# Performance work log

Hardware: AMD Instinct MI355X
Metric: run time of the kernel (lower is better)

The kernel has to match this reference:

```python
import jax, jax.numpy as jnp
import numpy as np

N_NODES = 100000
N_EDGES = 1600000
N_ROOTS = 2048


def _with_self_loops(edge_index, num_nodes):
    loop = jnp.arange(num_nodes, dtype=edge_index.dtype)
    src = jnp.concatenate([edge_index[0], loop])
    dst = jnp.concatenate([edge_index[1], loop])
    return src, dst


def gcn_conv(x, w, b, src, dst, num_nodes):
    xw = x @ w  # [N, Fout]
    deg = jax.ops.segment_sum(jnp.ones_like(dst, dtype=xw.dtype), dst,
                              num_segments=num_nodes)
    dinv = jnp.where(deg > 0, jax.lax.rsqrt(jnp.maximum(deg, 1.0)) * (deg > 0), 0.0)
    dinv = jnp.where(deg > 0, deg ** -0.5, 0.0)
    norm = dinv[src] * dinv[dst]  # [E+N]
    msgs = norm[:, None] * xw[src]  # [E+N, Fout] -- dominant memory traffic
    out = jax.ops.segment_sum(msgs, dst, num_segments=num_nodes)
    return out + b


def setup_inputs() -> dict:
    key = jax.random.key(0)
    ks = jax.random.split(key, 10)
    x = jax.random.normal(ks[0], (N_NODES, 256), dtype=jnp.float32)
    edge_index = jax.random.randint(ks[1], (2, N_EDGES), 0, N_NODES, dtype=jnp.int32)
    bu_edge_index = jax.random.randint(ks[2], (2, N_EDGES), 0, N_NODES, dtype=jnp.int32)
    rootindex = jax.random.randint(ks[3], (N_ROOTS,), 0, N_NODES, dtype=jnp.int32)
    def glorot(k, shape):
        lim = (6.0 / (shape[0] + shape[1])) ** 0.5
        return jax.random.uniform(k, shape, jnp.float32, -lim, lim)
    return {
        "x": x, "edge_index": edge_index, "bu_edge_index": bu_edge_index,
        "rootindex": rootindex,
        "w1": glorot(ks[4], (256, 128)), "b1": jnp.zeros((128,), jnp.float32),
        "w2": glorot(ks[5], (128, 128)), "b2": jnp.zeros((128,), jnp.float32),
        "w3": glorot(ks[6], (256, 128)), "b3": jnp.zeros((128,), jnp.float32),
        "w4": glorot(ks[7], (128, 128)), "b4": jnp.zeros((128,), jnp.float32),
        "fc_w": glorot(ks[8], (256, 4)), "fc_b": jnp.zeros((4,), jnp.float32),
    }


def reference(x, edge_index, bu_edge_index, rootindex,
              w1, b1, w2, b2, w3, b3, w4, b4, fc_w, fc_b):
    n = x.shape[0]
    src_td, dst_td = _with_self_loops(edge_index, n)
    src_bu, dst_bu = _with_self_loops(bu_edge_index, n)

    # Top-down branch (dropout is identity in eval mode)
    h = jax.nn.elu(gcn_conv(x, w1, b1, src_td, dst_td, n))
    h = jax.nn.elu(gcn_conv(h, w2, b2, src_td, dst_td, n))
    h = h[rootindex]  # [B, 128]

    # Bottom-up branch
    h1 = jax.nn.elu(gcn_conv(x, w3, b3, src_bu, dst_bu, n))
    h1 = jax.nn.elu(gcn_conv(h1, w4, b4, src_bu, dst_bu, n))
    h1 = h1[rootindex]  # [B, 128]

    feat = jnp.concatenate([h, h1], axis=1)  # [B, 256]
    logits = feat @ fc_w + fc_b  # [B, 4]
    return jax.nn.log_softmax(logits, axis=1)
```

## Files before the change

### kernel.cpp

```cpp
#include <hip/hip_runtime.h>
#include <hip/hip_fp16.h>
#include <math.h>

typedef __attribute__((ext_vector_type(8))) short short8v;
typedef __attribute__((ext_vector_type(4))) float float4v;
typedef __attribute__((ext_vector_type(4))) unsigned short ushort4v;
typedef __attribute__((ext_vector_type(8))) unsigned short ushort8v;

#define CH 4096
#define MAXNB 800

__device__ inline unsigned short f2bf(float f) {
    unsigned u = __float_as_uint(f);
    return (unsigned short)((u + 0x7FFFu + ((u >> 16) & 1u)) >> 16);
}


__global__ __launch_bounds__(256) void bin1_kernel(const int* __restrict__ dst, int E, int NB,
                                                   int* __restrict__ gcnt,
                                                   int* __restrict__ blockBase) {
    __shared__ int h[MAXNB];
    int t = threadIdx.x;
    for (int i = t; i < NB; i += 256) h[i] = 0;
    __syncthreads();
    int e0 = blockIdx.x * CH;
#pragma unroll
    for (int i = 0; i < CH / 256; ++i) {
        int e = e0 + t + i * 256;
        if (e < E) atomicAdd(&h[dst[e] >> 7], 1);
    }
    __syncthreads();
    for (int b = t; b < NB; b += 256) {
        int c = h[b];
        int old = atomicAdd(&gcnt[b], c);
        blockBase[(size_t)blockIdx.x * MAXNB + b] = old;
    }
}


__global__ void scan1_kernel(const int* __restrict__ cnt, int N,
                             int* __restrict__ offs) {
    __shared__ int sd[256];
    int t = threadIdx.x;
    int base = t * 4;
    int v[4]; int s = 0;
#pragma unroll
    for (int i = 0; i < 4; ++i) { v[i] = (base + i < N) ? cnt[base + i] : 0; s += v[i]; }
    sd[t] = s; __syncthreads();
    for (int d = 1; d < 256; d <<= 1) {
        int x = (t >= d) ? sd[t - d] : 0;
        __syncthreads();
        sd[t] += x;
        __syncthreads();
    }
    int p = sd[t] - s;
#pragma unroll
    for (int i = 0; i < 4; ++i) { if (base + i < N) offs[base + i] = p; p += v[i]; }
}


__global__ __launch_bounds__(256) void bin2_kernel(const int* __restrict__ src,
                                                   const int* __restrict__ dst, int E, int NB,
                                                   const int* __restrict__ boff,
                                                   const int* __restrict__ blockBase,
                                                   int* __restrict__ ebuf) {
    __shared__ int h[MAXNB];
    __shared__ int intra[MAXNB];
    __shared__ int cursor[MAXNB];
    __shared__ int gbase[MAXNB];
    __shared__ int ps[256];
    __shared__ int sorted[CH];
    __shared__ unsigned char sbkt[CH];
    int t = threadIdx.x;
    int blk = blockIdx.x;
    for (int i = t; i < NB; i += 256) h[i] = 0;
    __syncthreads();
    int e0 = blk * CH;
#pragma unroll
    for (int i = 0; i < CH / 256; ++i) {
        int e = e0 + t + i * 256;
        if (e < E) atomicAdd(&h[dst[e] >> 7], 1);
    }
    __syncthreads();
    int base4 = t * 4;
    int v[4]; int s = 0;
#pragma unroll
    for (int k = 0; k < 4; ++k) { v[k] = (base4 + k < NB) ? h[base4 + k] : 0; s += v[k]; }
    ps[t] = s; __syncthreads();
    for (int d = 1; d < 256; d <<= 1) {
        int x = (t >= d) ? ps[t - d] : 0;
        __syncthreads();
        ps[t] += x;
        __syncthreads();
    }
    int p = ps[t] - s;
#pragma unroll
    for (int k = 0; k < 4; ++k) { if (base4 + k < NB) intra[base4 + k] = p; p += v[k]; }
    __syncthreads();
    for (int b = t; b < NB; b += 256) {
        cursor[b] = intra[b];
        gbase[b] = boff[b] + blockBase[(size_t)blk * MAXNB + b] - intra[b];
    }
    __syncthreads();
#pragma unroll
    for (int i = 0; i < CH / 256; ++i) {
        int e = e0 + t + i * 256;
        if (e < E) {
            int d = dst[e];
            int b = d >> 7;
            int pos = atomicAdd(&cursor[b], 1);
            sorted[pos] = (src[e] << 7) | (d & 127);
            sbkt[pos] = (unsigned char)(b & 255);
        }
    }
    __syncthreads();
    int lim = E - e0; if (lim > CH) lim = CH;
    for (int i = t; i < lim; i += 256) {
        int pr = sorted[i];
        int lo = 0, hi = NB - 1;
        while (lo < hi) {
            int mid = (lo + hi + 1) >> 1;
            if (intra[mid] <= i) lo = mid; else hi = mid - 1;
        }
        ebuf[(size_t)gbase[lo] + i] = pr;
    }
}


__global__ __launch_bounds__(256) void csr_build_kernel(const int* __restrict__ ebuf,
                                                        const int* __restrict__ boff,
                                                        const int* __restrict__ gcnt,
                                                        int* __restrict__ csr,
                                                        int* __restrict__ offs,
                                                        int* __restrict__ cnt,
                                                        float* __restrict__ dinv, int N) {
    __shared__ int h[128];
    __shared__ int sc[128];
    __shared__ int loc[128];
    __shared__ int cur[128];
    int t = threadIdx.x, b = blockIdx.x;
    if (t < 128) h[t] = 0;
    __syncthreads();
    int o = boff[b], c = gcnt[b];
    for (int i = t; i < c; i += 256) atomicAdd(&h[ebuf[o + i] & 127], 1);
    __syncthreads();
    if (t < 128) sc[t] = h[t];
    __syncthreads();
    for (int d = 1; d < 128; d <<= 1) {
        int x = (t >= d && t < 128) ? sc[t - d] : 0;
        __syncthreads();
        if (t < 128) sc[t] += x;
        __syncthreads();
    }
    if (t < 128) { loc[t] = sc[t] - h[t]; cur[t] = loc[t]; }
    __syncthreads();
    for (int i = t; i < c; i += 256) {
        int pr = ebuf[o + i];
        int pos = atomicAdd(&cur[pr & 127], 1);
        csr[o + pos] = pr >> 7;
    }
    if (t < 128) {
        int v = b * 128 + t;
        if (v < N) {
            offs[v] = o + loc[t];
            cnt[v] = h[t];
            dinv[v] = rsqrtf((float)(h[t] + 1));
        }
    }
}


__global__ __launch_bounds__(256) void mark_kernel(const int* __restrict__ roots, int R,
                                                   const int* __restrict__ csr,
                                                   const int* __restrict__ offs,
                                                   const int* __restrict__ cnt,
                                                   unsigned char* __restrict__ flag) {
    int wid = (blockIdx.x * blockDim.x + threadIdx.x) >> 6;
    if (wid >= R) return;
    int lane = threadIdx.x & 63;
    int r = roots[wid];
    int o = offs[r], c = cnt[r];
    for (int i = lane; i < c; i += 64) flag[csr[o + i]] = 1;
    if (lane == 0) flag[r] = 1;
}

__global__ __launch_bounds__(256) void compact_kernel(const unsigned char* __restrict__ flag,
                                                      int N, int* __restrict__ nlist,
                                                      int* __restrict__ list,
                                                      int* __restrict__ inv) {
    int v = blockIdx.x * blockDim.x + threadIdx.x;
    if (v < N && flag[v]) {
        int p = atomicAdd(nlist, 1);
        list[p] = v;
        inv[v] = p;
    }
}


__global__ void wsplit_kernel(const float* __restrict__ W, int K,
                              unsigned short* __restrict__ WThi,
                              unsigned short* __restrict__ WTlo) {
    int i = blockIdx.x * blockDim.x + threadIdx.x;
    if (i >= K * 128) return;
    int k = i >> 7, c = i & 127;
    float w = W[i];
    unsigned short hh = f2bf(w);
    float hf = __uint_as_float((unsigned)hh << 16);
    WThi[(size_t)c * K + k] = hh;
    WTlo[(size_t)c * K + k] = f2bf(w - hf);
}


__global__ __launch_bounds__(256) void gemm_mfma_kernel(const float* __restrict__ A,
                                                        const unsigned short* __restrict__ WThi,
                                                        const unsigned short* __restrict__ WTlo,
                                                        __half* __restrict__ C, int M,
                                                        const int* __restrict__ Mdev, int K) {
    if (Mdev) M = *Mdev;
    int row0 = blockIdx.x * 128;
    if (row0 >= M) return;
    __shared__ unsigned short Ah[128 * 32];
    __shared__ unsigned short Al[128 * 32];
    __shared__ unsigned short Bh[128 * 32];
    __shared__ unsigned short Bl[128 * 32];
    int t = threadIdx.x;
    int w = t >> 6, l = t & 63;
    int lr = l & 15, lk = l >> 4;

    float4v acc[2][8];
#pragma unroll
    for (int mf = 0; mf < 2; ++mf)
#pragma unroll
        for (int nf = 0; nf < 8; ++nf) acc[mf][nf] = (float4v){0.f, 0.f, 0.f, 0.f};

    for (int k0 = 0; k0 < K; k0 += 32) {
#pragma unroll
        for (int i = 0; i < 4; ++i) {
            int idx = t + i * 256;
            int r = idx >> 3, c4 = (idx & 7) * 4;
            int gr = row0 + r;
            float4 v = {0.f, 0.f, 0.f, 0.f};
            if (gr < M) v = *(const float4*)(A + (size_t)gr * K + k0 + c4);
            float fs[4] = {v.x, v.y, v.z, v.w};
            ushort4v hi, lo;
#pragma unroll
            for (int j = 0; j < 4; ++j) {
                unsigned short hh = f2bf(fs[j]);
                float hf = __uint_as_float((unsigned)hh << 16);
                hi[j] = hh;
                lo[j] = f2bf(fs[j] - hf);
            }
            *(ushort4v*)&Ah[r * 32 + c4] = hi;
            *(ushort4v*)&Al[r * 32 + c4] = lo;
        }
#pragma unroll
        for (int i = 0; i < 2; ++i) {
            int cidx = t + i * 256;
            int col = cidx >> 2, q = cidx & 3;
            ushort8v vh = *(const ushort8v*)(WThi + (size_t)col * K + k0 + q * 8);
            ushort8v vl = *(const ushort8v*)(WTlo + (size_t)col * K + k0 + q * 8);
            *(ushort8v*)&Bh[col * 32 + q * 8] = vh;
            *(ushort8v*)&Bl[col * 32 + q * 8] = vl;
        }
        __syncthreads();

        short8v ah0 = *(const short8v*)&Ah[(w * 32 + lr) * 32 + lk * 8];
        short8v al0 = *(const short8v*)&Al[(w * 32 + lr) * 32 + lk * 8];
        short8v ah1 = *(const short8v*)&Ah[(w * 32 + 16 + lr) * 32 + lk * 8];
        short8v al1 = *(const short8v*)&Al[(w * 32 + 16 + lr) * 32 + lk * 8];
#pragma unroll
        for (int nf = 0; nf < 8; ++nf) {
            short8v bh = *(const short8v*)&Bh[(nf * 16 + lr) * 32 + lk * 8];
            short8v bl = *(const short8v*)&Bl[(nf * 16 + lr) * 32 + lk * 8];
            acc[0][nf] = __builtin_amdgcn_mfma_f32_16x16x32_bf16(ah0, bh, acc[0][nf], 0, 0, 0);
            acc[0][nf] = __builtin_amdgcn_mfma_f32_16x16x32_bf16(ah0, bl, acc[0][nf], 0, 0, 0);
            acc[0][nf] = __builtin_amdgcn_mfma_f32_16x16x32_bf16(al0, bh, acc[0][nf], 0, 0, 0);
            acc[1][nf] = __builtin_amdgcn_mfma_f32_16x16x32_bf16(ah1, bh, acc[1][nf], 0, 0, 0);
            acc[1][nf] = __builtin_amdgcn_mfma_f32_16x16x32_bf16(ah1, bl, acc[1][nf], 0, 0, 0);
            acc[1][nf] = __builtin_amdgcn_mfma_f32_16x16x32_bf16(al1, bh, acc[1][nf], 0, 0, 0);
        }
        __syncthreads();
    }
#pragma unroll
    for (int mf = 0; mf < 2; ++mf)
#pragma unroll
        for (int nf = 0; nf < 8; ++nf)
#pragma unroll
            for (int r = 0; r < 4; ++r) {
                int grow = row0 + w * 32 + mf * 16 + lk * 4 + r;
                if (grow < M) C[(size_t)grow * 128 + nf * 16 + lr] = __float2half(acc[mf][nf][r]);
            }
}


__global__ __launch_bounds__(256) void agg_kernel(const __half* __restrict__ xw,
                                                  const int* __restrict__ csr,
                                                  const int* __restrict__ offs,
                                                  const int* __restrict__ cnt,
                                                  const float* __restrict__ dinv,
                                                  const float* __restrict__ bias,
                                                  const int* __restrict__ nodelist,
                                                  const int* __restrict__ nwork_dev, int nwork,
                                                  float* __restrict__ out) {
    if (nwork_dev) nwork = *nwork_dev;
    int wid = (blockIdx.x * blockDim.x + threadIdx.x) >> 6;
    if (wid >= nwork) return;
    int lane = threadIdx.x & 63;
    int v = nodelist ? nodelist[wid] : wid;
    int o = offs[v];
    int c = cnt[v];
    float dv = dinv[v];
    float ax = 0.f, ay = 0.f;

    for (int base = 0; base < c; base += 64) {
        int rem = c - base; if (rem > 64) rem = 64;
        int li = base + lane; if (li >= c) li = c - 1;
        int s_l = csr[o + li];
        float d_l = dinv[s_l];
        int j = 0;
        for (; j + 4 <= rem; j += 4) {
            int s0 = __shfl(s_l, j);     int s1 = __shfl(s_l, j + 1);
            int s2 = __shfl(s_l, j + 2); int s3 = __shfl(s_l, j + 3);
            float e0 = __shfl(d_l, j);     float e1 = __shfl(d_l, j + 1);
            float e2 = __shfl(d_l, j + 2); float e3 = __shfl(d_l, j + 3);
            float2 v0 = __half22float2(*(const __half2*)(xw + (size_t)s0 * 128 + lane * 2));
            float2 v1 = __half22float2(*(const __half2*)(xw + (size_t)s1 * 128 + lane * 2));
            float2 v2 = __half22float2(*(const __half2*)(xw + (size_t)s2 * 128 + lane * 2));
            float2 v3 = __half22float2(*(const __half2*)(xw + (size_t)s3 * 128 + lane * 2));
            ax += e0 * v0.x + e1 * v1.x + e2 * v2.x + e3 * v3.x;
            ay += e0 * v0.y + e1 * v1.y + e2 * v2.y + e3 * v3.y;
        }
        for (; j < rem; ++j) {
            int s = __shfl(s_l, j);
            float e = __shfl(d_l, j);
            float2 vv = __half22float2(*(const __half2*)(xw + (size_t)s * 128 + lane * 2));
            ax += e * vv.x; ay += e * vv.y;
        }
    }
    float2 sv = __half22float2(*(const __half2*)(xw + (size_t)v * 128 + lane * 2));
    ax += dv * sv.x; ay += dv * sv.y;
    ax = dv * ax + bias[lane * 2];
    ay = dv * ay + bias[lane * 2 + 1];
    ax = ax > 0.f ? ax : expm1f(ax);
    ay = ay > 0.f ? ay : expm1f(ay);
    float2 res = {ax, ay};
    *(float2*)(out + (size_t)wid * 128 + lane * 2) = res;
}


__global__ __launch_bounds__(256) void root_agg_kernel(const __half* __restrict__ xwc,
                                                       const int* __restrict__ inv,
                                                       const int* __restrict__ csr,
                                                       const int* __restrict__ offs,
                                                       const int* __restrict__ cnt,
                                                       const float* __restrict__ dinv,
                                                       const float* __restrict__ bias,
                                                       const int* __restrict__ roots, int R,
                                                       float* __restrict__ feat, int col0) {
    int wid = (blockIdx.x * blockDim.x + threadIdx.x) >> 6;
    if (wid >= R) return;
    int lane = threadIdx.x & 63;
    int r = roots[wid];
    int o = offs[r], c = cnt[r];
    float dv = dinv[r];
    float ax = 0.f, ay = 0.f;
    for (int base = 0; base < c; base += 64) {
        int rem = c - base; if (rem > 64) rem = 64;
        int li = base + lane; if (li >= c) li = c - 1;
        int s_l = csr[o + li];
        float d_l = dinv[s_l];
        int iv_l = inv[s_l];
        for (int j = 0; j < rem; ++j) {
            int iv = __shfl(iv_l, j);
            float e = __shfl(d_l, j);
            float2 vv = __half22float2(*(const __half2*)(xwc + (size_t)iv * 128 + lane * 2));
            ax += e * vv.x; ay += e * vv.y;
        }
    }
    int ivr = inv[r];
    float2 sv = __half22float2(*(const __half2*)(xwc + (size_t)ivr * 128 + lane * 2));
    ax += dv * sv.x; ay += dv * sv.y;
    ax = dv * ax + bias[lane * 2];
    ay = dv * ay + bias[lane * 2 + 1];
    ax = ax > 0.f ? ax : expm1f(ax);
    ay = ay > 0.f ? ay : expm1f(ay);
    float2 res = {ax, ay};
    *(float2*)(feat + (size_t)wid * 256 + col0 + lane * 2) = res;
}


__global__ __launch_bounds__(256) void head_kernel(const float* __restrict__ feat,
                                                   const float* __restrict__ fcw,
                                                   const float* __restrict__ fcb,
                                                   float* __restrict__ out, int R) {
    int wid = (blockIdx.x * blockDim.x + threadIdx.x) >> 6;
    if (wid >= R) return;
    int lane = threadIdx.x & 63;
    const float* fr = feat + (size_t)wid * 256;
    float a0 = 0.f, a1 = 0.f, a2 = 0.f, a3 = 0.f;
    for (int k = lane; k < 256; k += 64) {
        float f = fr[k];
        float4 w = *(const float4*)(fcw + k * 4);
        a0 += f * w.x; a1 += f * w.y; a2 += f * w.z; a3 += f * w.w;
    }
#pragma unroll
    for (int d = 1; d < 64; d <<= 1) {
        a0 += __shfl_xor(a0, d); a1 += __shfl_xor(a1, d);
        a2 += __shfl_xor(a2, d); a3 += __shfl_xor(a3, d);
    }
    if (lane == 0) {
        a0 += fcb[0]; a1 += fcb[1]; a2 += fcb[2]; a3 += fcb[3];
        float m = fmaxf(fmaxf(a0, a1), fmaxf(a2, a3));
        float s = expf(a0 - m) + expf(a1 - m) + expf(a2 - m) + expf(a3 - m);
        float ls = logf(s) + m;
        float4 rr = {a0 - ls, a1 - ls, a2 - ls, a3 - ls};
        *(float4*)(out + (size_t)wid * 4) = rr;
    }
}


extern "C" void kernel_launch(void* const* d_in, const int* in_sizes, int n_in,
                              void* d_out, int out_size, void* d_ws, size_t ws_size,
                              hipStream_t stream) {
    const float* x    = (const float*)d_in[0];
    const int*   ei   = (const int*)d_in[1];
    const int*   bei  = (const int*)d_in[2];
    const int*   roots= (const int*)d_in[3];
    const float* w1 = (const float*)d_in[4];
    const float* b1 = (const float*)d_in[5];
    const float* w2 = (const float*)d_in[6];
    const float* b2 = (const float*)d_in[7];
    const float* w3 = (const float*)d_in[8];
    const float* b3 = (const float*)d_in[9];
    const float* w4 = (const float*)d_in[10];
    const float* b4 = (const float*)d_in[11];
    const float* fcw = (const float*)d_in[12];
    const float* fcb = (const float*)d_in[13];
    float* out = (float*)d_out;

    const int N = in_sizes[0] / 256;
    const int E = in_sizes[1] / 2;
    const int R = in_sizes[3];
    const int NB = (N + 127) >> 7;
    const int nblk = (E + CH - 1) / CH;

    char* ws = (char*)d_ws;
    size_t off = 0;
    auto alloc = [&](size_t b) { size_t o = off; off += (b + 255) & ~(size_t)255; return o; };
    __half* xw    = (__half*)(ws + alloc((size_t)N * 128 * 2));
    __half* xw2c  = (__half*)(ws + alloc((size_t)N * 128 * 2));
    float*  hc    = (float*)(ws + alloc((size_t)N * 128 * 4));
    int*   ebuf = (int*)(ws + alloc((size_t)E * 4));
    int*   csr  = (int*)(ws + alloc((size_t)E * 4));
    int*   blockBase = (int*)(ws + alloc((size_t)nblk * MAXNB * 4));
    int*   gcnt = (int*)(ws + alloc((size_t)MAXNB * 4));
    int*   boff = (int*)(ws + alloc((size_t)MAXNB * 4));
    int*   offs = (int*)(ws + alloc((size_t)N * 4));
    int*   cnt  = (int*)(ws + alloc((size_t)N * 4));
    float* dinv = (float*)(ws + alloc((size_t)N * 4));
    unsigned char* flag = (unsigned char*)(ws + alloc((size_t)N));
    int*   list = (int*)(ws + alloc((size_t)N * 4));
    int*   inv  = (int*)(ws + alloc((size_t)N * 4));
    int*   nlist = (int*)(ws + alloc(256));
    float* feat = (float*)(ws + alloc((size_t)R * 256 * 4));
    unsigned short* WThi = (unsigned short*)(ws + alloc((size_t)128 * 256 * 2));
    unsigned short* WTlo = (unsigned short*)(ws + alloc((size_t)128 * 256 * 2));

    for (int br = 0; br < 2; ++br) {
        const int* e    = (br == 0) ? ei : bei;
        const int* srcp = e;
        const int* dstp = e + E;
        const float* wA = (br == 0) ? w1 : w3;
        const float* bA = (br == 0) ? b1 : b3;
        const float* wB = (br == 0) ? w2 : w4;
        const float* bB = (br == 0) ? b2 : b4;

        hipMemsetAsync(gcnt, 0, (size_t)MAXNB * 4, stream);
        hipMemsetAsync(flag, 0, (size_t)N, stream);
        hipMemsetAsync(nlist, 0, 4, stream);
        bin1_kernel<<<nblk, 256, 0, stream>>>(dstp, E, NB, gcnt, blockBase);
        scan1_kernel<<<1, 256, 0, stream>>>(gcnt, NB, boff);
        bin2_kernel<<<nblk, 256, 0, stream>>>(srcp, dstp, E, NB, boff, blockBase, ebuf);
        csr_build_kernel<<<NB, 256, 0, stream>>>(ebuf, boff, gcnt, csr, offs, cnt, dinv, N);
        mark_kernel<<<(R * 64 + 255) / 256, 256, 0, stream>>>(roots, R, csr, offs, cnt, flag);
        compact_kernel<<<(N + 255) / 256, 256, 0, stream>>>(flag, N, nlist, list, inv);

        wsplit_kernel<<<(256 * 128 + 255) / 256, 256, 0, stream>>>(wA, 256, WThi, WTlo);
        gemm_mfma_kernel<<<(N + 127) / 128, 256, 0, stream>>>(x, WThi, WTlo, xw, N, nullptr, 256);
        agg_kernel<<<((size_t)N * 64 + 255) / 256, 256, 0, stream>>>(
            xw, csr, offs, cnt, dinv, bA, list, nlist, N, hc);
        wsplit_kernel<<<(128 * 128 + 255) / 256, 256, 0, stream>>>(wB, 128, WThi, WTlo);
        gemm_mfma_kernel<<<(N + 127) / 128, 256, 0, stream>>>(hc, WThi, WTlo, xw2c, N, nlist, 128);
        root_agg_kernel<<<((size_t)R * 64 + 255) / 256, 256, 0, stream>>>(
            xw2c, inv, csr, offs, cnt, dinv, bB, roots, R, feat, br * 128);
    }
    head_kernel<<<((size_t)R * 64 + 255) / 256, 256, 0, stream>>>(feat, fcw, fcb, out, R);
}
```

Baseline: 572.5 us.

## Fuse both branches' first-layer GEMMs into one dual-output kernel with swizzled LDS

```diff
diff --git a/kernel.cpp b/kernel.cpp
--- a/kernel.cpp
+++ b/kernel.cpp
@@ -4,11 +4,12 @@
 
 typedef __attribute__((ext_vector_type(8))) short short8v;
 typedef __attribute__((ext_vector_type(4))) float float4v;
-typedef __attribute__((ext_vector_type(4))) unsigned short ushort4v;
 typedef __attribute__((ext_vector_type(8))) unsigned short ushort8v;
 
 #define CH 4096
 #define MAXNB 800
+
+#define SWZ(row, ck) ((ck) ^ (((row) >> 1) & 3))
 
 __device__ inline unsigned short f2bf(float f) {
     unsigned u = __float_as_uint(f);
@@ -70,7 +71,6 @@
     __shared__ int gbase[MAXNB];
     __shared__ int ps[256];
     __shared__ int sorted[CH];
-    __shared__ unsigned char sbkt[CH];
     int t = threadIdx.x;
     int blk = blockIdx.x;
     for (int i = t; i < NB; i += 256) h[i] = 0;
@@ -110,7 +110,6 @@
             int b = d >> 7;
             int pos = atomicAdd(&cursor[b], 1);
             sorted[pos] = (src[e] << 7) | (d & 127);
-            sbkt[pos] = (unsigned char)(b & 255);
         }
     }
     __syncthreads();
@@ -208,6 +207,111 @@
     float hf = __uint_as_float((unsigned)hh << 16);
     WThi[(size_t)c * K + k] = hh;
     WTlo[(size_t)c * K + k] = f2bf(w - hf);
+}
+
+
+__global__ __launch_bounds__(256) void gemm1_dual_kernel(const float* __restrict__ A,
+                                                         const unsigned short* __restrict__ Bhi0,
+                                                         const unsigned short* __restrict__ Blo0,
+                                                         const unsigned short* __restrict__ Bhi1,
+                                                         const unsigned short* __restrict__ Blo1,
+                                                         __half* __restrict__ C0,
+                                                         __half* __restrict__ C1,
+                                                         int M, int K) {
+    __shared__ unsigned short Ah[128 * 32];
+    __shared__ unsigned short Al[128 * 32];
+    __shared__ unsigned short Bh[2][128 * 32];
+    __shared__ unsigned short Bl[2][128 * 32];
+    int t = threadIdx.x;
+    int w = t >> 6, l = t & 63;
+    int lr = l & 15, lk = l >> 4;
+    int row0 = blockIdx.x * 128;
+
+    float4v acc[2][2][8];
+#pragma unroll
+    for (int b = 0; b < 2; ++b)
+#pragma unroll
+        for (int mf = 0; mf < 2; ++mf)
+#pragma unroll
+            for (int nf = 0; nf < 8; ++nf) acc[b][mf][nf] = (float4v){0.f, 0.f, 0.f, 0.f};
+
+    for (int k0 = 0; k0 < K; k0 += 32) {
+#pragma unroll
+        for (int i = 0; i < 2; ++i) {
+            int idx = t + i * 256;
+            int r = idx >> 2, ck = idx & 3;
+            int gr = row0 + r;
+            float4 v0 = {0.f, 0.f, 0.f, 0.f}, v1 = {0.f, 0.f, 0.f, 0.f};
+            if (gr < M) {
+                const float* p = A + (size_t)gr * K + k0 + ck * 8;
+                v0 = *(const float4*)p;
+                v1 = *(const float4*)(p + 4);
+            }
+            float fs[8] = {v0.x, v0.y, v0.z, v0.w, v1.x, v1.y, v1.z, v1.w};
+            ushort8v hi, lo;
+#pragma unroll
+            for (int j = 0; j < 8; ++j) {
+                unsigned short hh = f2bf(fs[j]);
+                hi[j] = hh;
+                lo[j] = f2bf(fs[j] - __uint_as_float((unsigned)hh << 16));
+            }
+            int pos = r * 32 + SWZ(r, ck) * 8;
+            *(ushort8v*)&Ah[pos] = hi;
+            *(ushort8v*)&Al[pos] = lo;
+        }
+#pragma unroll
+        for (int i = 0; i < 2; ++i) {
+            int idx = t + i * 256;
+            int col = idx >> 2, ck = idx & 3;
+            size_t g = (size_t)col * K + k0 + ck * 8;
+            int pos = col * 32 + SWZ(col, ck) * 8;
+            *(ushort8v*)&Bh[0][pos] = *(const ushort8v*)(Bhi0 + g);
+            *(ushort8v*)&Bl[0][pos] = *(const ushort8v*)(Blo0 + g);
+            *(ushort8v*)&Bh[1][pos] = *(const ushort8v*)(Bhi1 + g);
+            *(ushort8v*)&Bl[1][pos] = *(const ushort8v*)(Blo1 + g);
+        }
+        __syncthreads();
+
+        int ar0 = w * 32 + lr, ar1 = w * 32 + 16 + lr;
+        short8v ah0 = *(const short8v*)&Ah[ar0 * 32 + SWZ(ar0, lk) * 8];
+        short8v al0 = *(const short8v*)&Al[ar0 * 32 + SWZ(ar0, lk) * 8];
+        short8v ah1 = *(const short8v*)&Ah[ar1 * 32 + SWZ(ar1, lk) * 8];
+        short8v al1 = *(const short8v*)&Al[ar1 * 32 + SWZ(ar1, lk) * 8];
+#pragma unroll
+        for (int nf = 0; nf < 8; ++nf) {
+            int brow = nf * 16 + lr;
+            int bpos = brow * 32 + SWZ(brow, lk) * 8;
+            short8v bh0 = *(const short8v*)&Bh[0][bpos];
+            short8v bl0 = *(const short8v*)&Bl[0][bpos];
+            acc[0][0][nf] = __builtin_amdgcn_mfma_f32_16x16x32_bf16(ah0, bh0, acc[0][0][nf], 0, 0, 0);
+            acc[0][0][nf] = __builtin_amdgcn_mfma_f32_16x16x32_bf16(ah0, bl0, acc[0][0][nf], 0, 0, 0);
+            acc[0][0][nf] = __builtin_amdgcn_mfma_f32_16x16x32_bf16(al0, bh0, acc[0][0][nf], 0, 0, 0);
+            acc[0][1][nf] = __builtin_amdgcn_mfma_f32_16x16x32_bf16(ah1, bh0, acc[0][1][nf], 0, 0, 0);
+            acc[0][1][nf] = __builtin_amdgcn_mfma_f32_16x16x32_bf16(ah1, bl0, acc[0][1][nf], 0, 0, 0);
+            acc[0][1][nf] = __builtin_amdgcn_mfma_f32_16x16x32_bf16(al1, bh0, acc[0][1][nf], 0, 0, 0);
+            short8v bh1 = *(const short8v*)&Bh[1][bpos];
+            short8v bl1 = *(const short8v*)&Bl[1][bpos];
+            acc[1][0][nf] = __builtin_amdgcn_mfma_f32_16x16x32_bf16(ah0, bh1, acc[1][0][nf], 0, 0, 0);
+            acc[1][0][nf] = __builtin_amdgcn_mfma_f32_16x16x32_bf16(ah0, bl1, acc[1][0][nf], 0, 0, 0);
+            acc[1][0][nf] = __builtin_amdgcn_mfma_f32_16x16x32_bf16(al0, bh1, acc[1][0][nf], 0, 0, 0);
+            acc[1][1][nf] = __builtin_amdgcn_mfma_f32_16x16x32_bf16(ah1, bh1, acc[1][1][nf], 0, 0, 0);
+            acc[1][1][nf] = __builtin_amdgcn_mfma_f32_16x16x32_bf16(ah1, bl1, acc[1][1][nf], 0, 0, 0);
+            acc[1][1][nf] = __builtin_amdgcn_mfma_f32_16x16x32_bf16(al1, bh1, acc[1][1][nf], 0, 0, 0);
+        }
+        __syncthreads();
+    }
+#pragma unroll
+    for (int mf = 0; mf < 2; ++mf)
+#pragma unroll
+        for (int nf = 0; nf < 8; ++nf)
+#pragma unroll
+            for (int r = 0; r < 4; ++r) {
+                int grow = row0 + w * 32 + mf * 16 + lk * 4 + r;
+                if (grow < M) {
+                    C0[(size_t)grow * 128 + nf * 16 + lr] = __float2half(acc[0][mf][nf][r]);
+                    C1[(size_t)grow * 128 + nf * 16 + lr] = __float2half(acc[1][mf][nf][r]);
+                }
+            }
 }
 
 
@@ -235,43 +339,50 @@
 
     for (int k0 = 0; k0 < K; k0 += 32) {
 #pragma unroll
-        for (int i = 0; i < 4; ++i) {
+        for (int i = 0; i < 2; ++i) {
             int idx = t + i * 256;
-            int r = idx >> 3, c4 = (idx & 7) * 4;
+            int r = idx >> 2, ck = idx & 3;
             int gr = row0 + r;
-            float4 v = {0.f, 0.f, 0.f, 0.f};
-            if (gr < M) v = *(const float4*)(A + (size_t)gr * K + k0 + c4);
-            float fs[4] = {v.x, v.y, v.z, v.w};
-            ushort4v hi, lo;
-#pragma unroll
-            for (int j = 0; j < 4; ++j) {
+            float4 v0 = {0.f, 0.f, 0.f, 0.f}, v1 = {0.f, 0.f, 0.f, 0.f};
+            if (gr < M) {
+                const float* p = A + (size_t)gr * K + k0 + ck * 8;
+                v0 = *(const float4*)p;
+                v1 = *(const float4*)(p + 4);
+            }
+            float fs[8] = {v0.x, v0.y, v0.z, v0.w, v1.x, v1.y, v1.z, v1.w};
+            ushort8v hi, lo;
+#pragma unroll
+            for (int j = 0; j < 8; ++j) {
                 unsigned short hh = f2bf(fs[j]);
-                float hf = __uint_as_float((unsigned)hh << 16);
                 hi[j] = hh;
-                lo[j] = f2bf(fs[j] - hf);
+                lo[j] = f2bf(fs[j] - __uint_as_float((unsigned)hh << 16));
             }
-            *(ushort4v*)&Ah[r * 32 + c4] = hi;
-            *(ushort4v*)&Al[r * 32 + c4] = lo;
+            int pos = r * 32 + SWZ(r, ck) * 8;
+            *(ushort8v*)&Ah[pos] = hi;
+            *(ushort8v*)&Al[pos] = lo;
         }
 #pragma unroll
         for (int i = 0; i < 2; ++i) {
-            int cidx = t + i * 256;
-            int col = cidx >> 2, q = cidx & 3;
-            ushort8v vh = *(const ushort8v*)(WThi + (size_t)col * K + k0 + q * 8);
-            ushort8v vl = *(const ushort8v*)(WTlo + (size_t)col * K + k0 + q * 8);
-            *(ushort8v*)&Bh[col * 32 + q * 8] = vh;
-            *(ushort8v*)&Bl[col * 32 + q * 8] = vl;
-        }
-        __syncthreads();
-
-        short8v ah0 = *(const short8v*)&Ah[(w * 32 + lr) * 32 + lk * 8];
-        short8v al0 = *(const short8v*)&Al[(w * 32 + lr) * 32 + lk * 8];
-        short8v ah1 = *(const short8v*)&Ah[(w * 32 + 16 + lr) * 32 + lk * 8];
-        short8v al1 = *(const short8v*)&Al[(w * 32 + 16 + lr) * 32 + lk * 8];
+            int idx = t + i * 256;
+            int col = idx >> 2, ck = idx & 3;
+            size_t g = (size_t)col * K + k0 + ck * 8;
+            int pos = col * 32 + SWZ(col, ck) * 8;
+            *(ushort8v*)&Bh[pos] = *(const ushort8v*)(WThi + g);
+            *(ushort8v*)&Bl[pos] = *(const ushort8v*)(WTlo + g);
+        }
+        __syncthreads();
+
+        int ar0 = w * 32 + lr, ar1 = w * 32 + 16 + lr;
+        short8v ah0 = *(const short8v*)&Ah[ar0 * 32 + SWZ(ar0, lk) * 8];
+        short8v al0 = *(const short8v*)&Al[ar0 * 32 + SWZ(ar0, lk) * 8];
+        short8v ah1 = *(const short8v*)&Ah[ar1 * 32 + SWZ(ar1, lk) * 8];
+        short8v al1 = *(const short8v*)&Al[ar1 * 32 + SWZ(ar1, lk) * 8];
 #pragma unroll
         for (int nf = 0; nf < 8; ++nf) {
-            short8v bh = *(const short8v*)&Bh[(nf * 16 + lr) * 32 + lk * 8];
-            short8v bl = *(const short8v*)&Bl[(nf * 16 + lr) * 32 + lk * 8];
+            int brow = nf * 16 + lr;
+            int bpos = brow * 32 + SWZ(brow, lk) * 8;
+            short8v bh = *(const short8v*)&Bh[bpos];
+            short8v bl = *(const short8v*)&Bl[bpos];
             acc[0][nf] = __builtin_amdgcn_mfma_f32_16x16x32_bf16(ah0, bh, acc[0][nf], 0, 0, 0);
             acc[0][nf] = __builtin_amdgcn_mfma_f32_16x16x32_bf16(ah0, bl, acc[0][nf], 0, 0, 0);
             acc[0][nf] = __builtin_amdgcn_mfma_f32_16x16x32_bf16(al0, bh, acc[0][nf], 0, 0, 0);
@@ -447,52 +558,72 @@
     char* ws = (char*)d_ws;
     size_t off = 0;
     auto alloc = [&](size_t b) { size_t o = off; off += (b + 255) & ~(size_t)255; return o; };
-    __half* xw    = (__half*)(ws + alloc((size_t)N * 128 * 2));
+    __half* xw0   = (__half*)(ws + alloc((size_t)N * 128 * 2));
+    __half* xw1   = (__half*)(ws + alloc((size_t)N * 128 * 2));
     __half* xw2c  = (__half*)(ws + alloc((size_t)N * 128 * 2));
     float*  hc    = (float*)(ws + alloc((size_t)N * 128 * 4));
     int*   ebuf = (int*)(ws + alloc((size_t)E * 4));
-    int*   csr  = (int*)(ws + alloc((size_t)E * 4));
     int*   blockBase = (int*)(ws + alloc((size_t)nblk * MAXNB * 4));
     int*   gcnt = (int*)(ws + alloc((size_t)MAXNB * 4));
     int*   boff = (int*)(ws + alloc((size_t)MAXNB * 4));
-    int*   offs = (int*)(ws + alloc((size_t)N * 4));
-    int*   cnt  = (int*)(ws + alloc((size_t)N * 4));
-    float* dinv = (float*)(ws + alloc((size_t)N * 4));
-    unsigned char* flag = (unsigned char*)(ws + alloc((size_t)N));
-    int*   list = (int*)(ws + alloc((size_t)N * 4));
-    int*   inv  = (int*)(ws + alloc((size_t)N * 4));
-    int*   nlist = (int*)(ws + alloc(256));
+    int*   csrA[2]; int* offsA[2]; int* cntA[2]; float* dinvA[2];
+    int*   listA[2]; int* invA[2]; int* nlistA[2];
+    unsigned char* flagA[2];
+    for (int br = 0; br < 2; ++br) {
+        csrA[br]  = (int*)(ws + alloc((size_t)E * 4));
+        offsA[br] = (int*)(ws + alloc((size_t)N * 4));
+        cntA[br]  = (int*)(ws + alloc((size_t)N * 4));
+        dinvA[br] = (float*)(ws + alloc((size_t)N * 4));
+        flagA[br] = (unsigned char*)(ws + alloc((size_t)N));
+        listA[br] = (int*)(ws + alloc((size_t)N * 4));
+        invA[br]  = (int*)(ws + alloc((size_t)N * 4));
+        nlistA[br]= (int*)(ws + alloc(256));
+    }
     float* feat = (float*)(ws + alloc((size_t)R * 256 * 4));
-    unsigned short* WThi = (unsigned short*)(ws + alloc((size_t)128 * 256 * 2));
-    unsigned short* WTlo = (unsigned short*)(ws + alloc((size_t)128 * 256 * 2));
+    unsigned short* WThi[4]; unsigned short* WTlo[4];
+    for (int i = 0; i < 4; ++i) {
+        int K = (i < 2) ? 256 : 128;
+        WThi[i] = (unsigned short*)(ws + alloc((size_t)128 * K * 2));
+        WTlo[i] = (unsigned short*)(ws + alloc((size_t)128 * K * 2));
+    }
 
     for (int br = 0; br < 2; ++br) {
         const int* e    = (br == 0) ? ei : bei;
         const int* srcp = e;
         const int* dstp = e + E;
-        const float* wA = (br == 0) ? w1 : w3;
-        const float* bA = (br == 0) ? b1 : b3;
-        const float* wB = (br == 0) ? w2 : w4;
-        const float* bB = (br == 0) ? b2 : b4;
-
         hipMemsetAsync(gcnt, 0, (size_t)MAXNB * 4, stream);
-        hipMemsetAsync(flag, 0, (size_t)N, stream);
-        hipMemsetAsync(nlist, 0, 4, stream);
+        hipMemsetAsync(flagA[br], 0, (size_t)N, stream);
+        hipMemsetAsync(nlistA[br], 0, 4, stream);
         bin1_kernel<<<nblk, 256, 0, stream>>>(dstp, E, NB, gcnt, blockBase);
         scan1_kernel<<<1, 256, 0, stream>>>(gcnt, NB, boff);
         bin2_kernel<<<nblk, 256, 0, stream>>>(srcp, dstp, E, NB, boff, blockBase, ebuf);
-        csr_build_kernel<<<NB, 256, 0, stream>>>(ebuf, boff, gcnt, csr, offs, cnt, dinv, N);
-        mark_kernel<<<(R * 64 + 255) / 256, 256, 0, stream>>>(roots, R, csr, offs, cnt, flag);
-        compact_kernel<<<(N + 255) / 256, 256, 0, stream>>>(flag, N, nlist, list, inv);
-
-        wsplit_kernel<<<(256 * 128 + 255) / 256, 256, 0, stream>>>(wA, 256, WThi, WTlo);
-        gemm_mfma_kernel<<<(N + 127) / 128, 256, 0, stream>>>(x, WThi, WTlo, xw, N, nullptr, 256);
+        csr_build_kernel<<<NB, 256, 0, stream>>>(ebuf, boff, gcnt, csrA[br], offsA[br],
+                                                 cntA[br], dinvA[br], N);
+        mark_kernel<<<(R * 64 + 255) / 256, 256, 0, stream>>>(roots, R, csrA[br], offsA[br],
+                                                              cntA[br], flagA[br]);
+        compact_kernel<<<(N + 255) / 256, 256, 0, stream>>>(flagA[br], N, nlistA[br],
+                                                            listA[br], invA[br]);
+    }
+
+    wsplit_kernel<<<(256 * 128 + 255) / 256, 256, 0, stream>>>(w1, 256, WThi[0], WTlo[0]);
+    wsplit_kernel<<<(256 * 128 + 255) / 256, 256, 0, stream>>>(w3, 256, WThi[1], WTlo[1]);
+    wsplit_kernel<<<(128 * 128 + 255) / 256, 256, 0, stream>>>(w2, 128, WThi[2], WTlo[2]);
+    wsplit_kernel<<<(128 * 128 + 255) / 256, 256, 0, stream>>>(w4, 128, WThi[3], WTlo[3]);
+
+    gemm1_dual_kernel<<<(N + 127) / 128, 256, 0, stream>>>(
+        x, WThi[0], WTlo[0], WThi[1], WTlo[1], xw0, xw1, N, 256);
+
+    for (int br = 0; br < 2; ++br) {
+        const __half* xwb = (br == 0) ? xw0 : xw1;
+        const float* bA = (br == 0) ? b1 : b3;
+        const float* bB = (br == 0) ? b2 : b4;
         agg_kernel<<<((size_t)N * 64 + 255) / 256, 256, 0, stream>>>(
-            xw, csr, offs, cnt, dinv, bA, list, nlist, N, hc);
-        wsplit_kernel<<<(128 * 128 + 255) / 256, 256, 0, stream>>>(wB, 128, WThi, WTlo);
-        gemm_mfma_kernel<<<(N + 127) / 128, 256, 0, stream>>>(hc, WThi, WTlo, xw2c, N, nlist, 128);
+            xwb, csrA[br], offsA[br], cntA[br], dinvA[br], bA, listA[br], nlistA[br], N, hc);
+        gemm_mfma_kernel<<<(N + 127) / 128, 256, 0, stream>>>(
+            hc, WThi[2 + br], WTlo[2 + br], xw2c, N, nlistA[br], 128);
         root_agg_kernel<<<((size_t)R * 64 + 255) / 256, 256, 0, stream>>>(
-            xw2c, inv, csr, offs, cnt, dinv, bB, roots, R, feat, br * 128);
+            xw2c, invA[br], csrA[br], offsA[br], cntA[br], dinvA[br], bB, roots, R,
+            feat, br * 128);
     }
     head_kernel<<<((size_t)R * 64 + 255) / 256, 256, 0, stream>>>(feat, fcw, fcb, out, R);
 }
```

Result: faster. 558.3 us (-2.5%).
